# Performance work log

Hardware: AMD Instinct MI355X
Metric: run time of the kernel (lower is better)

The kernel has to match this reference:

```python
import jax, jax.numpy as jnp
import numpy as np

NUM_HEADS = 4
SPLIT_SIZE = 8  # idx == 1 -> H_sp = H, W_sp = split_size (vertical stripe windows)


def setup_inputs() -> dict:
    key = jax.random.key(0)
    k1, k2, k3 = jax.random.split(key, 3)
    temp = jax.random.normal(k1, (16, 3, 128, 64, 64), dtype=jnp.float32)
    conv_w = jax.random.normal(k2, (128, 1, 3, 3), dtype=jnp.float32) * 0.1  # depthwise LePE conv
    conv_b = jax.random.normal(k3, (128,), dtype=jnp.float32) * 0.1
    return {"temp": temp, "conv_w": conv_w, "conv_b": conv_b}


def reference(temp, conv_w, conv_b):
    B, _, C, H, W = temp.shape
    H_sp, W_sp = H, SPLIT_SIZE          # idx == 1 cross-shaped window
    # H % H_sp == 0 and W % W_sp == 0 -> F.pad amounts are zero here
    nH, nW = H // H_sp, W // W_sp
    L = H_sp * W_sp                     # tokens per window
    hd = C // NUM_HEADS
    scale = hd ** -0.5

    q, k, v = temp[:, 0], temp[:, 1], temp[:, 2]  # each [B, C, H, W]

    def im2cswin(x):
        # img2windows: B C H W -> (B*nH*nW, L, C) then split heads -> (Bw, nh, L, hd)
        x = x.reshape(B, C, nH, H_sp, nW, W_sp).transpose(0, 2, 4, 3, 5, 1)
        x = x.reshape(-1, L, NUM_HEADS, hd).transpose(0, 2, 1, 3)
        return x

    qw = im2cswin(q) * scale            # (Bw, nh, L, hd)
    kw = im2cswin(k)

    # get_rpe: window-partition v as images, depthwise 3x3 conv for LePE
    vimg = v.reshape(B, C, nH, H_sp, nW, W_sp).transpose(0, 2, 4, 1, 3, 5)
    vimg = vimg.reshape(-1, C, H_sp, W_sp)  # (Bw, C, H_sp, W_sp)
    rpe = jax.lax.conv_general_dilated(
        vimg, conv_w, window_strides=(1, 1), padding="SAME",
        dimension_numbers=("NCHW", "OIHW", "NCHW"), feature_group_count=C,
    ) + conv_b[None, :, None, None]
    rpe = rpe.reshape(-1, NUM_HEADS, hd, L).transpose(0, 1, 3, 2)  # (Bw, nh, L, hd)
    vw = vimg.reshape(-1, NUM_HEADS, hd, L).transpose(0, 1, 3, 2)

    attn = jax.nn.softmax(jnp.einsum("wnld,wnmd->wnlm", qw, kw), axis=-1)
    out = jnp.einsum("wnlm,wnmd->wnld", attn, vw) + rpe  # (Bw, nh, L, hd)

    out = out.transpose(0, 2, 1, 3).reshape(-1, L, C)    # (Bw, L, C)
    # windows2img: (Bw, L, C) -> (B, H, W, C)
    out = out.reshape(B, nH, nW, H_sp, W_sp, C).transpose(0, 1, 3, 2, 4, 5)
    out = out.reshape(B, H, W, C)
    return out.reshape(B, H * W, C)
```

## Files before the change

### kernel.cpp

```cpp
#include <hip/hip_runtime.h>

typedef __attribute__((ext_vector_type(8))) short short8;
typedef __attribute__((ext_vector_type(4))) short short4_t;
typedef __attribute__((ext_vector_type(4))) float float4_t;
typedef __attribute__((ext_vector_type(4))) int int4_t;

#define CH_STRIDE 4096
#define IMG_STRIDE 524288
#define HW 4096
#define V520 520

static __device__ __forceinline__ short f2b(float x) {
    unsigned u = __builtin_bit_cast(unsigned, x);
    u = (u + 0x7fffu + ((u >> 16) & 1u)) >> 16;
    return (short)u;
}
static __device__ __forceinline__ float bitsf(unsigned u) { return __builtin_bit_cast(float, u); }
static __device__ __forceinline__ unsigned bitsu(float f) { return __builtin_bit_cast(unsigned, f); }

__global__ __launch_bounds__(512) void cswin_fused(
    const float* __restrict__ temp, const float* __restrict__ cw,
    const float* __restrict__ cb, float* __restrict__ out)
{
    __shared__ short Kc[64 * 40];
    __shared__ short Vt[32 * V520];

    int bx = blockIdx.x;
    int nw = bx >> 6;
    int r  = bx & 63;
    int b  = r >> 2;
    int n  = r & 3;

    int t    = threadIdx.x;
    int wv   = t >> 6;
    int lane = t & 63;
    int mr   = lane & 15;
    int q    = lane >> 4;

    const float* tq = temp + (size_t)b * 3 * IMG_STRIDE + (size_t)(n * 32) * CH_STRIDE + nw * 8;
    const float* tk = tq + IMG_STRIDE;
    const float* tv = tk + IMG_STRIDE;

    int row0 = wv * 64;
    const float qscale = 0.2550348889072310f;

    short8 Qf[4];
    #pragma unroll
    for (int qt = 0; qt < 4; ++qt) {
        int l = row0 + qt * 16 + mr;
        int sp = (l >> 3) * 64 + (l & 7);
        short8 f;
        #pragma unroll
        for (int j = 0; j < 8; ++j)
            f[j] = f2b(tq[(q * 8 + j) * CH_STRIDE + sp] * qscale);
        Qf[qt] = f;
    }

    float4_t zero4 = {0.f, 0.f, 0.f, 0.f};
    float4_t acc[2][4];
    #pragma unroll
    for (int dt = 0; dt < 2; ++dt)
        #pragma unroll
        for (int qt = 0; qt < 4; ++qt)
            acc[dt][qt] = zero4;
    float lsum[4] = {0.f, 0.f, 0.f, 0.f};

    int ld  = t >> 4;
    int seg = t & 15;
    const float* tkld = tk + (size_t)ld * CH_STRIDE;
    const float* tvld = tv + (size_t)ld * CH_STRIDE;

    int lb0 = seg * 4;
    int sp0 = (lb0 >> 3) * 64 + (lb0 & 7);
    float4_t k4 = *reinterpret_cast<const float4_t*>(tkld + sp0);
    float4_t v4 = *reinterpret_cast<const float4_t*>(tvld + sp0);

    int s0lane = (q & 1) * 32 + mr;
    int s1lane = s0lane + 16;
    bool hiq = (q >= 2);

    for (int ch = 0; ch < 8; ++ch) {
        __syncthreads();
        {
            int kl = seg * 4;
            Kc[(kl + 0) * 40 + ld] = f2b(k4.x);
            Kc[(kl + 1) * 40 + ld] = f2b(k4.y);
            Kc[(kl + 2) * 40 + ld] = f2b(k4.z);
            Kc[(kl + 3) * 40 + ld] = f2b(k4.w);
            short4_t vs = { f2b(v4.x), f2b(v4.y), f2b(v4.z), f2b(v4.w) };
            *reinterpret_cast<short4_t*>(&Vt[ld * V520 + ch * 64 + kl]) = vs;
        }
        if (ch < 7) {
            int lb = (ch + 1) * 64 + seg * 4;
            int sp = (lb >> 3) * 64 + (lb & 7);
            k4 = *reinterpret_cast<const float4_t*>(tkld + sp);
            v4 = *reinterpret_cast<const float4_t*>(tvld + sp);
        }
        __syncthreads();

        #pragma unroll
        for (int g = 0; g < 2; ++g) {
            short8 KaA = *reinterpret_cast<const short8*>(&Kc[((2 * g) * 16 + mr) * 40 + q * 8]);
            short8 KaB = *reinterpret_cast<const short8*>(&Kc[((2 * g + 1) * 16 + mr) * 40 + q * 8]);
            unsigned pa0[4], pa1[4], pb0[4], pb1[4];
            #pragma unroll
            for (int qt = 0; qt < 4; ++qt) {
                float4_t sA = __builtin_amdgcn_mfma_f32_16x16x32_bf16(KaA, Qf[qt], zero4, 0, 0, 0);
                float4_t sB = __builtin_amdgcn_mfma_f32_16x16x32_bf16(KaB, Qf[qt], zero4, 0, 0, 0);
                float eA0 = __builtin_amdgcn_exp2f(sA.x), eA1 = __builtin_amdgcn_exp2f(sA.y);
                float eA2 = __builtin_amdgcn_exp2f(sA.z), eA3 = __builtin_amdgcn_exp2f(sA.w);
                float eB0 = __builtin_amdgcn_exp2f(sB.x), eB1 = __builtin_amdgcn_exp2f(sB.y);
                float eB2 = __builtin_amdgcn_exp2f(sB.z), eB3 = __builtin_amdgcn_exp2f(sB.w);
                lsum[qt] += ((eA0 + eA1) + (eA2 + eA3)) + ((eB0 + eB1) + (eB2 + eB3));
                pa0[qt] = __builtin_amdgcn_perm(bitsu(eA1), bitsu(eA0), 0x07060302u);
                pa1[qt] = __builtin_amdgcn_perm(bitsu(eA3), bitsu(eA2), 0x07060302u);
                pb0[qt] = __builtin_amdgcn_perm(bitsu(eB1), bitsu(eB0), 0x07060302u);
                pb1[qt] = __builtin_amdgcn_perm(bitsu(eB3), bitsu(eB2), 0x07060302u);
            }
            int base = ch * 64 + g * 32 + q * 8;
            short8 Va0 = *reinterpret_cast<const short8*>(&Vt[mr * V520 + base]);
            short8 Va1 = *reinterpret_cast<const short8*>(&Vt[(16 + mr) * V520 + base]);
            #pragma unroll
            for (int qt = 0; qt < 4; ++qt) {
                int x0 = __shfl((int)pa0[qt], s0lane); int y0 = __shfl((int)pb0[qt], s0lane);
                int x1 = __shfl((int)pa1[qt], s0lane); int y1 = __shfl((int)pb1[qt], s0lane);
                int x2 = __shfl((int)pa0[qt], s1lane); int y2 = __shfl((int)pb0[qt], s1lane);
                int x3 = __shfl((int)pa1[qt], s1lane); int y3 = __shfl((int)pb1[qt], s1lane);
                int4_t pi = { hiq ? y0 : x0, hiq ? y1 : x1, hiq ? y2 : x2, hiq ? y3 : x3 };
                short8 Pb = __builtin_bit_cast(short8, pi);
                acc[0][qt] = __builtin_amdgcn_mfma_f32_16x16x32_bf16(Va0, Pb, acc[0][qt], 0, 0, 0);
                acc[1][qt] = __builtin_amdgcn_mfma_f32_16x16x32_bf16(Va1, Pb, acc[1][qt], 0, 0, 0);
            }
        }
    }

    float inv[4];
    #pragma unroll
    for (int qt = 0; qt < 4; ++qt) {
        float v = lsum[qt];
        v += __shfl_xor(v, 16);
        v += __shfl_xor(v, 32);
        inv[qt] = 1.0f / v;
    }

    float* outb = out + (size_t)b * HW * 128 + nw * 8 * 128 + n * 32;
    #pragma unroll
    for (int qt = 0; qt < 4; ++qt) {
        int l = row0 + qt * 16 + mr;
        size_t basep = (size_t)((l >> 3) * 64 + (l & 7)) * 128;
        #pragma unroll
        for (int dt = 0; dt < 2; ++dt) {
            float4_t o = acc[dt][qt] * inv[qt];
            *reinterpret_cast<float4_t*>(outb + basep + dt * 16 + q * 4) = o;
        }
    }

    __syncthreads();

    int c4 = (t & 7) * 4;
    int h  = t >> 3;
    float4_t outv[8];
    #pragma unroll
    for (int cc = 0; cc < 4; ++cc) {
        int c = c4 + cc;
        float w9[9];
        #pragma unroll
        for (int i = 0; i < 9; ++i) w9[i] = cw[(n * 32 + c) * 9 + i];
        float bias = cb[n * 32 + c];
        float rv[3][8];
        #pragma unroll
        for (int rr = 0; rr < 3; ++rr) {
            int hh = h - 1 + rr;
            if (hh >= 0 && hh < 64) {
                short8 u = *reinterpret_cast<const short8*>(&Vt[c * V520 + hh * 8]);
                #pragma unroll
                for (int j = 0; j < 8; ++j)
                    rv[rr][j] = bitsf(((unsigned)(unsigned short)u[j]) << 16);
            } else {
                #pragma unroll
                for (int j = 0; j < 8; ++j) rv[rr][j] = 0.f;
            }
        }
        #pragma unroll
        for (int w = 0; w < 8; ++w) {
            float o = bias;
            #pragma unroll
            for (int rr = 0; rr < 3; ++rr) {
                if (w > 0) o += rv[rr][w - 1] * w9[rr * 3 + 0];
                o += rv[rr][w] * w9[rr * 3 + 1];
                if (w < 7) o += rv[rr][w + 1] * w9[rr * 3 + 2];
            }
            outv[w][cc] = o;
        }
    }
    #pragma unroll
    for (int w = 0; w < 8; ++w) {
        size_t off = (size_t)h * 8192 + w * 128 + c4;
        float4_t cur = *reinterpret_cast<const float4_t*>(outb + off);
        cur += outv[w];
        *reinterpret_cast<float4_t*>(outb + off) = cur;
    }
}

extern "C" void kernel_launch(void* const* d_in, const int* in_sizes, int n_in,
                              void* d_out, int out_size, void* d_ws, size_t ws_size,
                              hipStream_t stream) {
    const float* temp = (const float*)d_in[0];
    const float* cw   = (const float*)d_in[1];
    const float* cb   = (const float*)d_in[2];
    float* out = (float*)d_out;
    hipLaunchKernelGGL(cswin_fused, dim3(512), dim3(512), 0, stream, temp, cw, cb, out);
}
```

Measured before the change: 191.6 us.

## Stage all K/V into shared memory upfront, removing per-chunk barriers

Result: slower. 205.0 us (+7.0%).

```diff
diff --git a/kernel.cpp b/kernel.cpp
--- a/kernel.cpp
+++ b/kernel.cpp
@@ -22,7 +22,7 @@
     const float* __restrict__ temp, const float* __restrict__ cw,
     const float* __restrict__ cb, float* __restrict__ out)
 {
-    __shared__ short Kc[64 * 40];
+    __shared__ short Kc[512 * 40];
     __shared__ short Vt[32 * V520];
 
     int bx = blockIdx.x;
@@ -44,6 +44,19 @@
     int row0 = wv * 64;
     const float qscale = 0.2550348889072310f;
 
+    int ld  = t & 31;
+    int seg = t >> 5;
+    const float* tkld = tk + (size_t)ld * CH_STRIDE;
+    const float* tvld = tv + (size_t)ld * CH_STRIDE;
+    float4_t kk[8], vv[8];
+    #pragma unroll
+    for (int rr = 0; rr < 8; ++rr) {
+        int lb = rr * 64 + seg * 4;
+        int sp = (lb >> 3) * 64 + (lb & 7);
+        kk[rr] = *reinterpret_cast<const float4_t*>(tkld + sp);
+        vv[rr] = *reinterpret_cast<const float4_t*>(tvld + sp);
+    }
+
     short8 Qf[4];
     #pragma unroll
     for (int qt = 0; qt < 4; ++qt) {
@@ -56,6 +69,17 @@
         Qf[qt] = f;
     }
 
+    #pragma unroll
+    for (int rr = 0; rr < 8; ++rr) {
+        int key = rr * 64 + seg * 4;
+        Kc[(key + 0) * 40 + ld] = f2b(kk[rr].x);
+        Kc[(key + 1) * 40 + ld] = f2b(kk[rr].y);
+        Kc[(key + 2) * 40 + ld] = f2b(kk[rr].z);
+        Kc[(key + 3) * 40 + ld] = f2b(kk[rr].w);
+        short4_t vs = { f2b(vv[rr].x), f2b(vv[rr].y), f2b(vv[rr].z), f2b(vv[rr].w) };
+        *reinterpret_cast<short4_t*>(&Vt[ld * V520 + key]) = vs;
+    }
+
     float4_t zero4 = {0.f, 0.f, 0.f, 0.f};
     float4_t acc[2][4];
     #pragma unroll
@@ -65,72 +89,43 @@
             acc[dt][qt] = zero4;
     float lsum[4] = {0.f, 0.f, 0.f, 0.f};
 
-    int ld  = t >> 4;
-    int seg = t & 15;
-    const float* tkld = tk + (size_t)ld * CH_STRIDE;
-    const float* tvld = tv + (size_t)ld * CH_STRIDE;
-
-    int lb0 = seg * 4;
-    int sp0 = (lb0 >> 3) * 64 + (lb0 & 7);
-    float4_t k4 = *reinterpret_cast<const float4_t*>(tkld + sp0);
-    float4_t v4 = *reinterpret_cast<const float4_t*>(tvld + sp0);
-
     int s0lane = (q & 1) * 32 + mr;
     int s1lane = s0lane + 16;
     bool hiq = (q >= 2);
 
-    for (int ch = 0; ch < 8; ++ch) {
-        __syncthreads();
-        {
-            int kl = seg * 4;
-            Kc[(kl + 0) * 40 + ld] = f2b(k4.x);
-            Kc[(kl + 1) * 40 + ld] = f2b(k4.y);
-            Kc[(kl + 2) * 40 + ld] = f2b(k4.z);
-            Kc[(kl + 3) * 40 + ld] = f2b(k4.w);
-            short4_t vs = { f2b(v4.x), f2b(v4.y), f2b(v4.z), f2b(v4.w) };
-            *reinterpret_cast<short4_t*>(&Vt[ld * V520 + ch * 64 + kl]) = vs;
-        }
-        if (ch < 7) {
-            int lb = (ch + 1) * 64 + seg * 4;
-            int sp = (lb >> 3) * 64 + (lb & 7);
-            k4 = *reinterpret_cast<const float4_t*>(tkld + sp);
-            v4 = *reinterpret_cast<const float4_t*>(tvld + sp);
-        }
-        __syncthreads();
-
-        #pragma unroll
-        for (int g = 0; g < 2; ++g) {
-            short8 KaA = *reinterpret_cast<const short8*>(&Kc[((2 * g) * 16 + mr) * 40 + q * 8]);
-            short8 KaB = *reinterpret_cast<const short8*>(&Kc[((2 * g + 1) * 16 + mr) * 40 + q * 8]);
-            unsigned pa0[4], pa1[4], pb0[4], pb1[4];
-            #pragma unroll
-            for (int qt = 0; qt < 4; ++qt) {
-                float4_t sA = __builtin_amdgcn_mfma_f32_16x16x32_bf16(KaA, Qf[qt], zero4, 0, 0, 0);
-                float4_t sB = __builtin_amdgcn_mfma_f32_16x16x32_bf16(KaB, Qf[qt], zero4, 0, 0, 0);
-                float eA0 = __builtin_amdgcn_exp2f(sA.x), eA1 = __builtin_amdgcn_exp2f(sA.y);
-                float eA2 = __builtin_amdgcn_exp2f(sA.z), eA3 = __builtin_amdgcn_exp2f(sA.w);
-                float eB0 = __builtin_amdgcn_exp2f(sB.x), eB1 = __builtin_amdgcn_exp2f(sB.y);
-                float eB2 = __builtin_amdgcn_exp2f(sB.z), eB3 = __builtin_amdgcn_exp2f(sB.w);
-                lsum[qt] += ((eA0 + eA1) + (eA2 + eA3)) + ((eB0 + eB1) + (eB2 + eB3));
-                pa0[qt] = __builtin_amdgcn_perm(bitsu(eA1), bitsu(eA0), 0x07060302u);
-                pa1[qt] = __builtin_amdgcn_perm(bitsu(eA3), bitsu(eA2), 0x07060302u);
-                pb0[qt] = __builtin_amdgcn_perm(bitsu(eB1), bitsu(eB0), 0x07060302u);
-                pb1[qt] = __builtin_amdgcn_perm(bitsu(eB3), bitsu(eB2), 0x07060302u);
-            }
-            int base = ch * 64 + g * 32 + q * 8;
-            short8 Va0 = *reinterpret_cast<const short8*>(&Vt[mr * V520 + base]);
-            short8 Va1 = *reinterpret_cast<const short8*>(&Vt[(16 + mr) * V520 + base]);
-            #pragma unroll
-            for (int qt = 0; qt < 4; ++qt) {
-                int x0 = __shfl((int)pa0[qt], s0lane); int y0 = __shfl((int)pb0[qt], s0lane);
-                int x1 = __shfl((int)pa1[qt], s0lane); int y1 = __shfl((int)pb1[qt], s0lane);
-                int x2 = __shfl((int)pa0[qt], s1lane); int y2 = __shfl((int)pb0[qt], s1lane);
-                int x3 = __shfl((int)pa1[qt], s1lane); int y3 = __shfl((int)pb1[qt], s1lane);
-                int4_t pi = { hiq ? y0 : x0, hiq ? y1 : x1, hiq ? y2 : x2, hiq ? y3 : x3 };
-                short8 Pb = __builtin_bit_cast(short8, pi);
-                acc[0][qt] = __builtin_amdgcn_mfma_f32_16x16x32_bf16(Va0, Pb, acc[0][qt], 0, 0, 0);
-                acc[1][qt] = __builtin_amdgcn_mfma_f32_16x16x32_bf16(Va1, Pb, acc[1][qt], 0, 0, 0);
-            }
+    __syncthreads();
+
+    for (int gg = 0; gg < 16; ++gg) {
+        short8 KaA = *reinterpret_cast<const short8*>(&Kc[(gg * 32 + mr) * 40 + q * 8]);
+        short8 KaB = *reinterpret_cast<const short8*>(&Kc[(gg * 32 + 16 + mr) * 40 + q * 8]);
+        unsigned pa0[4], pa1[4], pb0[4], pb1[4];
+        #pragma unroll
+        for (int qt = 0; qt < 4; ++qt) {
+            float4_t sA = __builtin_amdgcn_mfma_f32_16x16x32_bf16(KaA, Qf[qt], zero4, 0, 0, 0);
+            float4_t sB = __builtin_amdgcn_mfma_f32_16x16x32_bf16(KaB, Qf[qt], zero4, 0, 0, 0);
+            float eA0 = __builtin_amdgcn_exp2f(sA.x), eA1 = __builtin_amdgcn_exp2f(sA.y);
+            float eA2 = __builtin_amdgcn_exp2f(sA.z), eA3 = __builtin_amdgcn_exp2f(sA.w);
+            float eB0 = __builtin_amdgcn_exp2f(sB.x), eB1 = __builtin_amdgcn_exp2f(sB.y);
+            float eB2 = __builtin_amdgcn_exp2f(sB.z), eB3 = __builtin_amdgcn_exp2f(sB.w);
+            lsum[qt] += ((eA0 + eA1) + (eA2 + eA3)) + ((eB0 + eB1) + (eB2 + eB3));
+            pa0[qt] = __builtin_amdgcn_perm(bitsu(eA1), bitsu(eA0), 0x07060302u);
+            pa1[qt] = __builtin_amdgcn_perm(bitsu(eA3), bitsu(eA2), 0x07060302u);
+            pb0[qt] = __builtin_amdgcn_perm(bitsu(eB1), bitsu(eB0), 0x07060302u);
+            pb1[qt] = __builtin_amdgcn_perm(bitsu(eB3), bitsu(eB2), 0x07060302u);
+        }
+        int base = gg * 32 + q * 8;
+        short8 Va0 = *reinterpret_cast<const short8*>(&Vt[mr * V520 + base]);
+        short8 Va1 = *reinterpret_cast<const short8*>(&Vt[(16 + mr) * V520 + base]);
+        #pragma unroll
+        for (int qt = 0; qt < 4; ++qt) {
+            int x0 = __shfl((int)pa0[qt], s0lane); int y0 = __shfl((int)pb0[qt], s0lane);
+            int x1 = __shfl((int)pa1[qt], s0lane); int y1 = __shfl((int)pb1[qt], s0lane);
+            int x2 = __shfl((int)pa0[qt], s1lane); int y2 = __shfl((int)pb0[qt], s1lane);
+            int x3 = __shfl((int)pa1[qt], s1lane); int y3 = __shfl((int)pb1[qt], s1lane);
+            int4_t pi = { hiq ? y0 : x0, hiq ? y1 : x1, hiq ? y2 : x2, hiq ? y3 : x3 };
+            short8 Pb = __builtin_bit_cast(short8, pi);
+            acc[0][qt] = __builtin_amdgcn_mfma_f32_16x16x32_bf16(Va0, Pb, acc[0][qt], 0, 0, 0);
+            acc[1][qt] = __builtin_amdgcn_mfma_f32_16x16x32_bf16(Va1, Pb, acc[1][qt], 0, 0, 0);
         }
     }
 
```
